# Performance work log

Hardware: AMD Instinct MI355X
Metric: run time of the kernel (lower is better)

The kernel has to match this reference:

```python
import jax, jax.numpy as jnp
import numpy as np

D = 256      # input_dim
SE = 512     # emo seq len
SC = 512     # cause seq len
CKS = 8      # chunksize
KC = 3       # causes per emo utterance


def _linear(k, fi, fo):
    kw, kb = jax.random.split(k)
    bound = 1.0 / np.sqrt(fi)
    w = jax.random.uniform(kw, (fi, fo), jnp.float32, -bound, bound)
    b = jax.random.uniform(kb, (fo,), jnp.float32, -bound, bound)
    return w, b


def setup_inputs() -> dict:
    key = jax.random.key(0)
    ks = jax.random.split(key, 12)
    text_emo = jax.random.normal(ks[0], (SE, 1, D), jnp.float32)
    text_cau = jax.random.normal(ks[1], (SC, 1, D), jnp.float32)
    label_ck = jnp.ones((SE, SC // CKS), jnp.int64 if jax.config.jax_enable_x64 else jnp.int32)
    label3 = jax.random.randint(ks[2], (SE, 1, KC), 0, SC)
    rep_W, rep_b = _linear(ks[3], D, D)
    W_W, W_b = _linear(ks[4], 2 * D, D)
    Wo_W, Wo_b = _linear(ks[5], D, 2)
    # GRU params, torch layout transposed to (in, 3*hidden); gate order r,z,n
    bound = 1.0 / np.sqrt(D)
    gru_Wih = jax.random.uniform(ks[6], (D, 3 * D), jnp.float32, -bound, bound)
    gru_Whh = jax.random.uniform(ks[7], (D, 3 * D), jnp.float32, -bound, bound)
    gru_bih = jax.random.uniform(ks[8], (3 * D,), jnp.float32, -bound, bound)
    gru_bhh = jax.random.uniform(ks[9], (3 * D,), jnp.float32, -bound, bound)
    W3_W, W3_b = _linear(ks[10], 3 * D + 1, D)
    cls_W, cls_b = _linear(ks[11], D, 2)
    return {"text_emo": text_emo, "text_cau": text_cau, "label_ck": label_ck,
            "label3": label3, "chunksize": CKS,
            "rep_W": rep_W, "rep_b": rep_b, "W_W": W_W, "W_b": W_b,
            "Wo_W": Wo_W, "Wo_b": Wo_b,
            "gru_Wih": gru_Wih, "gru_Whh": gru_Whh,
            "gru_bih": gru_bih, "gru_bhh": gru_bhh,
            "W3_W": W3_W, "W3_b": W3_b, "cls_W": cls_W, "cls_b": cls_b}


def reference(text_emo, text_cau, label_ck, label3, chunksize,
              rep_W, rep_b, W_W, W_b, Wo_W, Wo_b,
              gru_Wih, gru_Whh, gru_bih, gru_bhh,
              W3_W, W3_b, cls_W, cls_b):
    d = text_emo.shape[-1]
    # shared representation: relu(Linear)
    te = jax.nn.relu(text_emo @ rep_W + rep_b)   # (SE,1,d)
    tc = jax.nn.relu(text_cau @ rep_W + rep_b)   # (SC,1,d)
    emo = te[:, 0, :]                             # (SE,d) batch==1
    cau = tc[:, 0, :]                             # (SC,d)
    se, sc = emo.shape[0], cau.shape[0]
    C = sc // chunksize
    chunks = cau.reshape(C, chunksize, d)         # torch.split of text_cau

    # GRU over each chunk with zero initial state; take last hidden.
    # (Original re-runs this identically for every emo timestep; math is the same.)
    def gru_last(ch):
        def step(h, x):
            gx = x @ gru_Wih + gru_bih
            gh = h @ gru_Whh + gru_bhh
            xr, xz, xn = jnp.split(gx, 3)
            hr, hz, hn = jnp.split(gh, 3)
            r = jax.nn.sigmoid(xr + hr)
            z = jax.nn.sigmoid(xz + hz)
            n = jnp.tanh(xn + r * hn)
            return (1.0 - z) * n + z * h, None
        h, _ = jax.lax.scan(step, jnp.zeros((d,), ch.dtype), ch)
        return h
    ch_last = jax.vmap(gru_last)(chunks)          # (C,d)

    # phase 2: chunk-level classifier per emo timestep (dropout = identity, eval)
    chunkEmb = jnp.concatenate([
        jnp.broadcast_to(emo[:, None, :], (se, C, d)),
        jnp.broadcast_to(ch_last[None, :, :], (se, C, d))], axis=-1)  # (SE,C,2d)
    hidden = jax.nn.sigmoid(chunkEmb @ W_W + W_b)
    phase2 = jax.nn.log_softmax(hidden @ Wo_W + Wo_b, axis=-1)        # (SE,C,2)

    # phase 3: t_ratio=1 -> idx = label_ck[j]; label_ck all ones selects every
    # chunk, so utt_c == full text_cau for each emo step.
    item2 = jnp.linalg.norm(emo[:, None, :] - cau[None, :, :], axis=-1, keepdims=True)
    delta = jnp.concatenate([
        jnp.broadcast_to(emo[:, None, :], (se, sc, d)),
        jnp.broadcast_to(cau[None, :, :], (se, sc, d)),
        item2,
        emo[:, None, :] * cau[None, :, :]], axis=-1)   # (SE,SC,3d+1)
    h3 = jax.nn.relu(delta @ W3_W + W3_b)
    p = jax.nn.log_softmax(h3 @ cls_W + cls_b, axis=-1)               # (SE,SC,2)

    # label3_out: per emo step, binary cause vector over cause utterances
    lab3 = label3[:, 0, :]                                            # (SE,KC)
    L_cau = jnp.zeros((se, sc), phase2.dtype).at[
        jnp.arange(se)[:, None], lab3].set(1.0)
    return phase2, p, L_cau
```

## Files before the change

kernel.cpp:

```cpp
#include <hip/hip_runtime.h>
#include <hip/hip_bf16.h>
#include <hip/hip_fp16.h>
#include <math.h>

#define D   256
#define SE  512
#define SC  512
#define CKS 8
#define NC  64
#define KC  3

typedef __attribute__((ext_vector_type(8))) short short8_t;
typedef __attribute__((ext_vector_type(4))) float f32x4;
typedef _Float16 h2_t __attribute__((ext_vector_type(2)));
typedef _Float16 h8_t __attribute__((ext_vector_type(8)));

__device__ __forceinline__ float sigmoidf_(float x) { return 1.f / (1.f + __expf(-x)); }
__device__ __forceinline__ short bf16s(float f) {
    union { __hip_bfloat16 h; short s; } u; u.h = __float2bfloat16(f); return u.s;
}
__device__ __forceinline__ float bflo(unsigned int u) {
    union { unsigned int u; float f; } v; v.u = u << 16; return v.f;
}
__device__ __forceinline__ short h16s(float f) {
    union { _Float16 h; short s; } u; u.h = (_Float16)f; return u.s;
}
__device__ __forceinline__ float h16f(short s) {
    union { short s; _Float16 h; } u; u.s = s; return (float)u.h;
}
__device__ __forceinline__ h2_t h2u(unsigned int u) {
    union { unsigned int u; h2_t h; } v; v.u = u; return v.h;
}
__device__ __forceinline__ unsigned int u2h(h2_t h) {
    union { unsigned int u; h2_t h; } v; v.h = h; return v.u;
}
__device__ __forceinline__ float hdot2(h2_t a, h2_t b, float c) {
#if __has_builtin(__builtin_amdgcn_fdot2)
    return __builtin_amdgcn_fdot2(a, b, c, false);
#else
    h2_t p = a * b;
    return c + (float)p[0] + (float)p[1];
#endif
}
#define GLOAD_LDS16(g, l) \
    __builtin_amdgcn_global_load_lds((const __attribute__((address_space(1))) void*)(g), \
                                     (__attribute__((address_space(3))) void*)(l), 16, 0, 0)

__global__ __launch_bounds__(256) void prep_all_kernel(
    const float* __restrict__ W3, const float* __restrict__ Wih,
    const float* __restrict__ Whh, const float* __restrict__ WW,
    const float* __restrict__ repW, const float* __restrict__ clsW,
    short* __restrict__ Bprep, uint2* __restrict__ Wih16, uint2* __restrict__ Whh16,
    float4* __restrict__ WWq, float4* __restrict__ W3q,
    float4* __restrict__ repWq, unsigned int* __restrict__ clsP)
{
    const int b = blockIdx.x, t = threadIdx.x;
    if (b < 32) {
        const int idx = b * 256 + t;
        const int p = idx >> 11, k = (idx >> 3) & 255, G = idx & 7;
        const int dbase = p * 64 + ((G ^ (k & 7)) << 3);
        #pragma unroll
        for (int e = 0; e < 8; ++e)
            Bprep[idx * 8 + e] = h16s(W3[(size_t)(513 + dbase + e) * D + k]);
    } else if (b < 416) {
        const bool ih = (b < 224);
        const int tid = (b - (ih ? 32 : 224)) * 256 + t;
        const float* W = ih ? Wih : Whh;
        const int base = (tid / 768) * 4 * 768 + (tid % 768);
        float f0 = W[base], f1 = W[base + 768], f2 = W[base + 1536], f3 = W[base + 2304];
        __half2 plo = __halves2half2(__float2half_rn(f0), __float2half_rn(f1));
        __half2 phi = __halves2half2(__float2half_rn(f2), __float2half_rn(f3));
        uint2 o; o.x = *(unsigned int*)&plo; o.y = *(unsigned int*)&phi;
        (ih ? Wih16 : Whh16)[tid] = o;
    } else if (b < 672) {
        const bool ww = (b < 544);
        const int tid = (b - (ww ? 416 : 544)) * 256 + t;
        const int h = tid >> 14, rem = tid & 16383, d4 = rem >> 8, k = rem & 255;
        const float* src = (ww ? WW : W3) + (size_t)(h * 256 + 4 * d4) * D + k;
        (ww ? WWq : W3q)[tid] = make_float4(src[0], src[256], src[512], src[768]);
    } else if (b < 736) {
        const int tid = (b - 672) * 256 + t;
        const int d4 = tid >> 8, k = tid & 255;
        const float* src = repW + (size_t)(4 * d4) * D + k;
        repWq[tid] = make_float4(src[0], src[256], src[512], src[768]);
    } else {
        unsigned int c0 = (unsigned int)(unsigned short)bf16s(clsW[t * 2]);
        unsigned int c1 = (unsigned int)(unsigned short)bf16s(clsW[t * 2 + 1]);
        clsP[t] = c0 | (c1 << 16);
    }
}

__global__ __launch_bounds__(256) void rep4_kernel(
    const float* __restrict__ te, const float* __restrict__ tc,
    const float4* __restrict__ repWq, const float* __restrict__ b,
    float* __restrict__ emo, float* __restrict__ cau,
    short* __restrict__ emoH, short* __restrict__ cauH,
    float* __restrict__ se2, float* __restrict__ sc2)
{
    const int r0 = blockIdx.x * 4, t = threadIdx.x;
    const float* X = (r0 < SE) ? (te + (size_t)r0 * D) : (tc + (size_t)(r0 - SE) * D);
    __shared__ __align__(16) float xs[4][D];
    #pragma unroll
    for (int r = 0; r < 4; ++r) xs[r][t] = X[r * D + t];
    __syncthreads();
    float acc0 = 0.f, acc1 = 0.f, acc2 = 0.f, acc3 = 0.f;
    #pragma unroll 8
    for (int q = 0; q < 64; ++q) {
        float4 w = repWq[q * 256 + t];
        float4 x0 = *(const float4*)&xs[0][q * 4];
        float4 x1 = *(const float4*)&xs[1][q * 4];
        float4 x2 = *(const float4*)&xs[2][q * 4];
        float4 x3 = *(const float4*)&xs[3][q * 4];
        acc0 = fmaf(x0.x, w.x, acc0); acc0 = fmaf(x0.y, w.y, acc0); acc0 = fmaf(x0.z, w.z, acc0); acc0 = fmaf(x0.w, w.w, acc0);
        acc1 = fmaf(x1.x, w.x, acc1); acc1 = fmaf(x1.y, w.y, acc1); acc1 = fmaf(x1.z, w.z, acc1); acc1 = fmaf(x1.w, w.w, acc1);
        acc2 = fmaf(x2.x, w.x, acc2); acc2 = fmaf(x2.y, w.y, acc2); acc2 = fmaf(x2.z, w.z, acc2); acc2 = fmaf(x2.w, w.w, acc2);
        acc3 = fmaf(x3.x, w.x, acc3); acc3 = fmaf(x3.y, w.y, acc3); acc3 = fmaf(x3.z, w.z, acc3); acc3 = fmaf(x3.w, w.w, acc3);
    }
    const float bb = b[t];
    float v[4] = {fmaxf(acc0 + bb, 0.f), fmaxf(acc1 + bb, 0.f), fmaxf(acc2 + bb, 0.f), fmaxf(acc3 + bb, 0.f)};
    short hv[4];
    #pragma unroll
    for (int r = 0; r < 4; ++r) hv[r] = h16s(v[r]);
    #pragma unroll
    for (int r = 0; r < 4; ++r) {
        const int row = r0 + r;
        if (row < SE) { emo[(size_t)row * D + t] = v[r]; emoH[(size_t)row * D + t] = hv[r]; }
        else { cau[(size_t)(row - SE) * D + t] = v[r]; cauH[(size_t)(row - SE) * D + t] = hv[r]; }
    }
    __shared__ float rsum[4][4];
    #pragma unroll
    for (int r = 0; r < 4; ++r) {
        const float f = h16f(hv[r]);
        float s = f * f;
        s += __shfl_xor(s, 1);  s += __shfl_xor(s, 2);
        s += __shfl_xor(s, 4);  s += __shfl_xor(s, 8);
        s += __shfl_xor(s, 16); s += __shfl_xor(s, 32);
        if ((t & 63) == 0) rsum[r][t >> 6] = s;
    }
    __syncthreads();
    if (t < 4) {
        const float tot = rsum[t][0] + rsum[t][1] + rsum[t][2] + rsum[t][3];
        const int row = r0 + t;
        if (row < SE) se2[row] = tot; else sc2[row - SE] = tot;
    }
}

__global__ __launch_bounds__(768) void gx2_kernel(
    const float* __restrict__ cau, const uint2* __restrict__ Wih16,
    const float* __restrict__ bih, __half* __restrict__ GX16)
{
    const int r0 = blockIdx.x * 2, t = threadIdx.x;
    __shared__ uint2 xs4[2][64];
    if (t < 128) {
        const int r = t >> 6, c = t & 63;
        float4 v = *(const float4*)&cau[(size_t)(r0 + r) * D + c * 4];
        __half2 plo = __halves2half2(__float2half_rn(v.x), __float2half_rn(v.y));
        __half2 phi = __halves2half2(__float2half_rn(v.z), __float2half_rn(v.w));
        uint2 o; o.x = *(unsigned int*)&plo; o.y = *(unsigned int*)&phi;
        xs4[r][c] = o;
    }
    __syncthreads();
    __half2 a00 = __float2half2_rn(0.f), a01 = __float2half2_rn(0.f);
    __half2 a10 = __float2half2_rn(0.f), a11 = __float2half2_rn(0.f);
    #pragma unroll 8
    for (int q = 0; q < 64; ++q) {
        uint2 w = Wih16[q * 768 + t];
        uint2 x0 = xs4[0][q], x1 = xs4[1][q];
        a00 = __hfma2(*(__half2*)&w.x, *(__half2*)&x0.x, a00);
        a01 = __hfma2(*(__half2*)&w.y, *(__half2*)&x0.y, a01);
        a10 = __hfma2(*(__half2*)&w.x, *(__half2*)&x1.x, a10);
        a11 = __hfma2(*(__half2*)&w.y, *(__half2*)&x1.y, a11);
    }
    const float bi = bih[t];
    float g0 = bi + __low2float(a00) + __high2float(a00) + __low2float(a01) + __high2float(a01);
    float g1 = bi + __low2float(a10) + __high2float(a10) + __low2float(a11) + __high2float(a11);
    GX16[(size_t)r0 * 768 + t] = __float2half_rn(g0);
    GX16[(size_t)(r0 + 1) * 768 + t] = __float2half_rn(g1);
}

__global__ __launch_bounds__(768) void gru_rec_kernel(
    const __half* __restrict__ GX16, const uint2* __restrict__ Whh16,
    const float* __restrict__ bhh, float* __restrict__ ch_last)
{
    const int c = blockIdx.x, t = threadIdx.x;
    __shared__ uint2 hqu[64];
    __shared__ float gh_s[768];
    uint2 wreg[64];
    #pragma unroll
    for (int q = 0; q < 64; ++q) wreg[q] = Whh16[q * 768 + t];
    float h = 0.f;
    if (t < 64) { uint2 z; z.x = 0u; z.y = 0u; hqu[t] = z; }
    __syncthreads();
    const float bh = bhh[t];
    for (int s = 0; s < CKS; ++s) {
        const int row = c * CKS + s;
        __half2 a0 = __float2half2_rn(0.f), a1 = __float2half2_rn(0.f);
        #pragma unroll
        for (int q = 0; q < 64; ++q) {
            uint2 hv = hqu[q];
            a0 = __hfma2(*(__half2*)&wreg[q].x, *(__half2*)&hv.x, a0);
            a1 = __hfma2(*(__half2*)&wreg[q].y, *(__half2*)&hv.y, a1);
        }
        gh_s[t] = bh + __low2float(a0) + __high2float(a0) + __low2float(a1) + __high2float(a1);
        __syncthreads();
        if (t < 256) {
            const float gxr = __half2float(GX16[(size_t)row * 768 + t]);
            const float gxz = __half2float(GX16[(size_t)row * 768 + 256 + t]);
            const float gxn = __half2float(GX16[(size_t)row * 768 + 512 + t]);
            float r = sigmoidf_(gxr + gh_s[t]);
            float z = sigmoidf_(gxz + gh_s[256 + t]);
            float n = tanhf(gxn + r * gh_s[512 + t]);
            h = (1.f - z) * n + z * h;
            float f1 = __shfl_down(h, 1);
            float f2 = __shfl_down(h, 2);
            float f3 = __shfl_down(h, 3);
            if ((t & 3) == 0) {
                __half2 plo = __halves2half2(__float2half_rn(h),  __float2half_rn(f1));
                __half2 phi = __halves2half2(__float2half_rn(f2), __float2half_rn(f3));
                uint2 o; o.x = *(unsigned int*)&plo; o.y = *(unsigned int*)&phi;
                hqu[t >> 2] = o;
            }
        }
        __syncthreads();
    }
    if (t < 256) ch_last[c * D + t] = h;
}

__global__ __launch_bounds__(256) void dual_all4_kernel(
    const float* __restrict__ emo, const float* __restrict__ cau, const float* __restrict__ chl,
    const float4* __restrict__ WWq, const float4* __restrict__ W3q,
    const float* __restrict__ Wb, const float* __restrict__ W3b,
    float* __restrict__ HE, float* __restrict__ HC, float* __restrict__ Ae,
    short* __restrict__ AcB)
{
    const int r0 = blockIdx.x * 4, t = threadIdx.x;
    const float* X; const float4* Wq; float bias;
    int seg;
    if (r0 < 512)       { X = emo + (size_t)r0 * D;          Wq = WWq;         bias = 0.f;    seg = 0; }
    else if (r0 < 576)  { X = chl + (size_t)(r0 - 512) * D;  Wq = WWq + 16384; bias = Wb[t];  seg = 1; }
    else if (r0 < 1088) { X = emo + (size_t)(r0 - 576) * D;  Wq = W3q;         bias = 0.f;    seg = 2; }
    else                { X = cau + (size_t)(r0 - 1088) * D; Wq = W3q + 16384; bias = W3b[t]; seg = 3; }
    __shared__ __align__(16) float xs[4][D];
    #pragma unroll
    for (int r = 0; r < 4; ++r) xs[r][t] = X[r * D + t];
    __syncthreads();
    float a0 = bias, a1 = bias, a2 = bias, a3 = bias;
    #pragma unroll 8
    for (int q = 0; q < 64; ++q) {
        float4 w = Wq[q * 256 + t];
        float4 x0 = *(const float4*)&xs[0][q * 4];
        float4 x1 = *(const float4*)&xs[1][q * 4];
        float4 x2 = *(const float4*)&xs[2][q * 4];
        float4 x3 = *(const float4*)&xs[3][q * 4];
        a0 = fmaf(x0.x, w.x, a0); a0 = fmaf(x0.y, w.y, a0); a0 = fmaf(x0.z, w.z, a0); a0 = fmaf(x0.w, w.w, a0);
        a1 = fmaf(x1.x, w.x, a1); a1 = fmaf(x1.y, w.y, a1); a1 = fmaf(x1.z, w.z, a1); a1 = fmaf(x1.w, w.w, a1);
        a2 = fmaf(x2.x, w.x, a2); a2 = fmaf(x2.y, w.y, a2); a2 = fmaf(x2.z, w.z, a2); a2 = fmaf(x2.w, w.w, a2);
        a3 = fmaf(x3.x, w.x, a3); a3 = fmaf(x3.y, w.y, a3); a3 = fmaf(x3.z, w.z, a3); a3 = fmaf(x3.w, w.w, a3);
    }
    float av[4] = {a0, a1, a2, a3};
    #pragma unroll
    for (int r = 0; r < 4; ++r) {
        const int row = r0 + r;
        if (seg == 0)      HE[(size_t)row * D + t] = av[r];
        else if (seg == 1) HC[(size_t)(row - 512) * D + t] = av[r];
        else if (seg == 2) Ae[(size_t)(row - 576) * D + t] = av[r];
        else               AcB[(size_t)(row - 1088) * D + t] = bf16s(av[r]);
    }
}

__global__ __launch_bounds__(256) void phase2_kernel(
    const float* __restrict__ HE, const float* __restrict__ HC,
    const float* __restrict__ WoW, const float* __restrict__ Wob,
    float* __restrict__ out)
{
    const int i = blockIdx.x, t = threadIdx.x;
    const int c = t >> 2, sub = t & 3;
    __shared__ __align__(16) float he_s[D];
    he_s[t] = HE[(size_t)i * D + t];
    __syncthreads();
    float v0 = 0.f, v1 = 0.f;
    const float* hcRow = HC + (size_t)c * D;
    #pragma unroll 4
    for (int kk = 0; kk < 16; ++kk) {
        const int k4 = sub * 64 + kk * 4;
        float4 he = *(const float4*)&he_s[k4];
        float4 hc = *(const float4*)&hcRow[k4];
        float hk;
        hk = sigmoidf_(he.x + hc.x); { float2 wo = *(const float2*)&WoW[(k4 + 0) * 2]; v0 = fmaf(hk, wo.x, v0); v1 = fmaf(hk, wo.y, v1); }
        hk = sigmoidf_(he.y + hc.y); { float2 wo = *(const float2*)&WoW[(k4 + 1) * 2]; v0 = fmaf(hk, wo.x, v0); v1 = fmaf(hk, wo.y, v1); }
        hk = sigmoidf_(he.z + hc.z); { float2 wo = *(const float2*)&WoW[(k4 + 2) * 2]; v0 = fmaf(hk, wo.x, v0); v1 = fmaf(hk, wo.y, v1); }
        hk = sigmoidf_(he.w + hc.w); { float2 wo = *(const float2*)&WoW[(k4 + 3) * 2]; v0 = fmaf(hk, wo.x, v0); v1 = fmaf(hk, wo.y, v1); }
    }
    v0 += __shfl_xor(v0, 1); v0 += __shfl_xor(v0, 2);
    v1 += __shfl_xor(v1, 1); v1 += __shfl_xor(v1, 2);
    if (sub == 0) {
        float l0 = v0 + Wob[0], l1 = v1 + Wob[1];
        float m = fmaxf(l0, l1);
        float lse = m + __logf(__expf(l0 - m) + __expf(l1 - m));
        float2 o; o.x = l0 - lse; o.y = l1 - lse;
        *(float2*)&out[((size_t)i * NC + c) * 2] = o;
    }
}

__global__ __launch_bounds__(512) void p_kernel(
    const short* __restrict__ emoH, const float* __restrict__ se2, const float* __restrict__ sc2,
    const float* __restrict__ Ae,  const short* __restrict__ AcB,
    const float* __restrict__ wn,  const short* __restrict__ Bprep,
    const short* __restrict__ cauH, const float* __restrict__ clsW,
    float* __restrict__ pp)
{
    const int t = threadIdx.x;
    const int i0 = blockIdx.x * 8;
    const int jt = blockIdx.y >> 1, kh = blockIdx.y & 1;
    const int j0 = jt * 64;
    const int l = t & 63, wave = t >> 6;
    const int hi = l >> 4, lo = l & 15;
    const int wj = wave >> 1, wk = wave & 1;
    const int j_base = wj * 16, k_base = wk * 64;
    const int myj = j0 + j_base + lo;

    __shared__ __align__(16) short B_s[32768];
    __shared__ float part2[64][2][2];

    #pragma unroll
    for (int r = 0; r < 8; ++r) {
        const int g = r * 512 + t;
        const int p = g >> 10, rem = g & 1023;
        GLOAD_LDS16(Bprep + ((size_t)(p * 256 + kh * 128) * 8 + rem) * 8, &B_s[g * 8]);
    }

    int kcol[4]; float wn_r[4], c0_r[4], c1_r[4];
    #pragma unroll
    for (int kf = 0; kf < 4; ++kf) {
        const int kg = kh * 128 + k_base + kf * 16 + lo;
        kcol[kf] = kg;
        wn_r[kf] = wn[kg];
        c0_r[kf] = clsW[kg * 2]; c1_r[kf] = clsW[kg * 2 + 1];
    }
    const int swzf0 = (hi ^ (lo & 7)) << 3;
    const int swzf1 = ((4 + hi) ^ (lo & 7)) << 3;
    const float sc2_l = sc2[myj];
    float Ac_r[4][4];
    #pragma unroll
    for (int q = 0; q < 4; ++q)
        #pragma unroll
        for (int kf = 0; kf < 4; ++kf)
            Ac_r[q][kf] = bflo((unsigned int)(unsigned short)AcB[(size_t)(j0 + j_base + hi * 4 + q) * D + kcol[kf]]);

    uint4 cfr[8];
    #pragma unroll
    for (int s = 0; s < 8; ++s) {
        const int p = s >> 1, df = s & 1;
        cfr[s] = *(const uint4*)&cauH[(size_t)myj * D + p * 64 + (df * 4 + hi) * 8];
    }
    __syncthreads();

    #pragma unroll 1
    for (int ii = 0; ii < 8; ii += 2) {
        __syncthreads();
        f32x4 acc[2][4];
        #pragma unroll
        for (int u = 0; u < 2; ++u)
            #pragma unroll
            for (int kf = 0; kf < 4; ++kf) acc[u][kf] = (f32x4)(0.f);
        float dot0 = 0.f, dot1 = 0.f;

        #pragma unroll
        for (int s = 0; s < 8; ++s) {
            const int p = s >> 1, df = s & 1;
            const uint4 eu0 = *(const uint4*)&emoH[(size_t)(i0 + ii) * D + p * 64 + (df * 4 + hi) * 8];
            const uint4 eu1 = *(const uint4*)&emoH[(size_t)(i0 + ii + 1) * D + p * 64 + (df * 4 + hi) * 8];
            const uint4 cu = cfr[s];
            const h2_t c0 = h2u(cu.x), c1 = h2u(cu.y), c2 = h2u(cu.z), c3 = h2u(cu.w);
            const h2_t a0 = h2u(eu0.x), a1 = h2u(eu0.y), a2 = h2u(eu0.z), a3 = h2u(eu0.w);
            const h2_t b0 = h2u(eu1.x), b1 = h2u(eu1.y), b2 = h2u(eu1.z), b3 = h2u(eu1.w);
            dot0 = hdot2(a0, c0, dot0); dot0 = hdot2(a1, c1, dot0);
            dot0 = hdot2(a2, c2, dot0); dot0 = hdot2(a3, c3, dot0);
            dot1 = hdot2(b0, c0, dot1); dot1 = hdot2(b1, c1, dot1);
            dot1 = hdot2(b2, c2, dot1); dot1 = hdot2(b3, c3, dot1);
            union { uint4 u; h8_t h; } af0, af1;
            af0.u.x = u2h(a0 * c0); af0.u.y = u2h(a1 * c1);
            af0.u.z = u2h(a2 * c2); af0.u.w = u2h(a3 * c3);
            af1.u.x = u2h(b0 * c0); af1.u.y = u2h(b1 * c1);
            af1.u.z = u2h(b2 * c2); af1.u.w = u2h(b3 * c3);
            const int swz = df ? swzf1 : swzf0;
            #pragma unroll
            for (int kf = 0; kf < 4; ++kf) {
                const h8_t bf = *(const h8_t*)&B_s[p * 8192 + (k_base + kf * 16 + lo) * 64 + swz];
                acc[0][kf] = __builtin_amdgcn_mfma_f32_16x16x32_f16(af0.h, bf, acc[0][kf], 0, 0, 0);
                acc[1][kf] = __builtin_amdgcn_mfma_f32_16x16x32_f16(af1.h, bf, acc[1][kf], 0, 0, 0);
            }
        }

        #pragma unroll
        for (int u = 0; u < 2; ++u) {
            const int i = i0 + ii + u;
            float dv = u ? dot1 : dot0;
            dv += __shfl_xor(dv, 16); dv += __shfl_xor(dv, 32);
            const float itv_own = sqrtf(fmaxf(se2[i] + sc2_l - 2.f * dv, 0.f));
            float Ae_r[4];
            #pragma unroll
            for (int kf = 0; kf < 4; ++kf) Ae_r[kf] = Ae[(size_t)i * D + kcol[kf]];
            if (u) __syncthreads();
            #pragma unroll
            for (int q = 0; q < 4; ++q) {
                const int j = j_base + hi * 4 + q;
                const float itv = __shfl(itv_own, hi * 4 + q);
                float sv0 = 0.f, sv1 = 0.f;
                #pragma unroll
                for (int kf = 0; kf < 4; ++kf) {
                    float s = acc[u][kf][q] + Ae_r[kf] + Ac_r[q][kf] + itv * wn_r[kf];
                    float h = fmaxf(s, 0.f);
                    sv0 = fmaf(h, c0_r[kf], sv0); sv1 = fmaf(h, c1_r[kf], sv1);
                }
                sv0 += __shfl_xor(sv0, 1); sv0 += __shfl_xor(sv0, 2);
                sv0 += __shfl_xor(sv0, 4); sv0 += __shfl_xor(sv0, 8);
                sv1 += __shfl_xor(sv1, 1); sv1 += __shfl_xor(sv1, 2);
                sv1 += __shfl_xor(sv1, 4); sv1 += __shfl_xor(sv1, 8);
                if (lo == 0) { part2[j][wk][0] = sv0; part2[j][wk][1] = sv1; }
            }
            __syncthreads();
            if (t < 64) {
                float2 o;
                o.x = part2[t][0][0] + part2[t][1][0];
                o.y = part2[t][0][1] + part2[t][1][1];
                *(float2*)&pp[(((size_t)kh * SE + i) * SC + j0 + t) * 2] = o;
            }
        }
    }
}

__global__ __launch_bounds__(512) void pfin_kernel(
    const float* __restrict__ pp, const float* __restrict__ clsb,
    float* __restrict__ pout)
{
    const int i = blockIdx.x, j = threadIdx.x;
    const float2 a = *(const float2*)&pp[((size_t)i * SC + j) * 2];
    const float2 b = *(const float2*)&pp[(((size_t)SE + i) * SC + j) * 2];
    float s0 = a.x + b.x + clsb[0];
    float s1 = a.y + b.y + clsb[1];
    float m = fmaxf(s0, s1);
    float lse = m + __logf(__expf(s0 - m) + __expf(s1 - m));
    float2 o; o.x = s0 - lse; o.y = s1 - lse;
    *(float2*)&pout[((size_t)i * SC + j) * 2] = o;
}

__global__ __launch_bounds__(128) void lcau_kernel(const int* __restrict__ label3, float* __restrict__ L)
{
    const int row = blockIdx.x, t = threadIdx.x;
    float4 z; z.x = z.y = z.z = z.w = 0.f;
    *(float4*)&L[(size_t)row * SC + t * 4] = z;
    __syncthreads();
    if (t < KC) {
        int j = label3[row * KC + t];
        L[(size_t)row * SC + j] = 1.0f;
    }
}

extern "C" void kernel_launch(void* const* d_in, const int* in_sizes, int n_in,
                              void* d_out, int out_size, void* d_ws, size_t ws_size,
                              hipStream_t stream)
{
    const float* text_emo = (const float*)d_in[0];
    const float* text_cau = (const float*)d_in[1];
    const int*   label3   = (const int*)d_in[3];
    const float* rep_W = (const float*)d_in[5];
    const float* rep_b = (const float*)d_in[6];
    const float* W_W   = (const float*)d_in[7];
    const float* W_b   = (const float*)d_in[8];
    const float* Wo_W  = (const float*)d_in[9];
    const float* Wo_b  = (const float*)d_in[10];
    const float* gWih  = (const float*)d_in[11];
    const float* gWhh  = (const float*)d_in[12];
    const float* gbih  = (const float*)d_in[13];
    const float* gbhh  = (const float*)d_in[14];
    const float* W3_W  = (const float*)d_in[15];
    const float* W3_b  = (const float*)d_in[16];
    const float* cls_W = (const float*)d_in[17];
    const float* cls_b = (const float*)d_in[18];

    float* out        = (float*)d_out;
    float* phase2_out = out;
    float* p_out      = out + SE * NC * 2;
    float* lcau_out   = out + SE * NC * 2 + SE * SC * 2;

    float* ws  = (float*)d_ws;
    float* emo = ws;
    float* cau = emo + 131072;
    float* chl = cau + 131072;
    float* HE  = chl + 16384;
    float* HC  = HE + 131072;
    float* Ae  = HC + 16384;
    float4* WWq = (float4*)(Ae + 131072);
    float4* W3q = WWq + 32768;
    short* AcB   = (short*)(W3q + 32768);
    short* Bprep = AcB + 131072;
    uint2* Wih16 = (uint2*)(Bprep + 65536);
    uint2* Whh16 = Wih16 + 49152;
    float4* repWq = (float4*)(Whh16 + 49152);
    short* cauH = (short*)(repWq + 16384);
    short* emoH = cauH + 131072;
    unsigned int* clsP = (unsigned int*)(emoH + 131072);
    float* pp = (float*)(clsP + 256);
    float* sc2 = pp + 1048576;
    float* se2 = sc2 + 512;
    __half* GX16 = (__half*)HE;

    prep_all_kernel<<<737, 256, 0, stream>>>(W3_W, gWih, gWhh, W_W, rep_W, cls_W,
                                             Bprep, Wih16, Whh16, WWq, W3q, repWq, clsP);
    rep4_kernel<<<256, 256, 0, stream>>>(text_emo, text_cau, repWq, rep_b, emo, cau,
                                         emoH, cauH, se2, sc2);
    gx2_kernel<<<256, 768, 0, stream>>>(cau, Wih16, gbih, GX16);
    gru_rec_kernel<<<NC, 768, 0, stream>>>(GX16, Whh16, gbhh, chl);
    dual_all4_kernel<<<400, 256, 0, stream>>>(emo, cau, chl, WWq, W3q, W_b, W3_b,
                                              HE, HC, Ae, AcB);
    phase2_kernel<<<SE, 256, 0, stream>>>(HE, HC, Wo_W, Wo_b, phase2_out);
    p_kernel<<<dim3(64, 16), 512, 0, stream>>>(emoH, se2, sc2, Ae, AcB, W3_W + 512 * D,
                                               Bprep, cauH, cls_W, pp);
    pfin_kernel<<<SE, 512, 0, stream>>>(pp, cls_b, p_out);
    lcau_kernel<<<SE, 128, 0, stream>>>(label3, lcau_out);
}
```

Before: 172.1 us.

## Process one emo row per p_kernel iteration and fuse L_cau into pfin kernel

The p_kernel main loop now handles one emotion row per iteration instead of two. Each cause fragment's MFMA B-operand load from shared memory therefore feeds one MFMA rather than two, but accumulator registers drop by half. The separate lcau kernel is merged into the log-softmax finalisation kernel, which removes one launch. The order of two FMAs in the rep kernel is also swapped, which slightly changes rounding.

```diff
diff --git a/kernel.cpp b/kernel.cpp
--- a/kernel.cpp
+++ b/kernel.cpp
@@ -114,7 +114,7 @@
         acc0 = fmaf(x0.x, w.x, acc0); acc0 = fmaf(x0.y, w.y, acc0); acc0 = fmaf(x0.z, w.z, acc0); acc0 = fmaf(x0.w, w.w, acc0);
         acc1 = fmaf(x1.x, w.x, acc1); acc1 = fmaf(x1.y, w.y, acc1); acc1 = fmaf(x1.z, w.z, acc1); acc1 = fmaf(x1.w, w.w, acc1);
         acc2 = fmaf(x2.x, w.x, acc2); acc2 = fmaf(x2.y, w.y, acc2); acc2 = fmaf(x2.z, w.z, acc2); acc2 = fmaf(x2.w, w.w, acc2);
-        acc3 = fmaf(x3.x, w.x, acc3); acc3 = fmaf(x3.y, w.y, acc3); acc3 = fmaf(x3.z, w.z, acc3); acc3 = fmaf(x3.w, w.w, acc3);
+        acc3 = fmaf(x3.x, w.x, acc3); acc3 = fmaf(x3.y, w.y, acc3); acc3 = fmaf(x3.w, w.w, acc3); acc3 = fmaf(x3.z, w.z, acc3);
     }
     const float bb = b[t];
     float v[4] = {fmaxf(acc0 + bb, 0.f), fmaxf(acc1 + bb, 0.f), fmaxf(acc2 + bb, 0.f), fmaxf(acc3 + bb, 0.f)};
@@ -356,83 +356,76 @@
     __syncthreads();
 
     #pragma unroll 1
-    for (int ii = 0; ii < 8; ii += 2) {
+    for (int ii = 0; ii < 8; ++ii) {
+        const int i = i0 + ii;
         __syncthreads();
-        f32x4 acc[2][4];
-        #pragma unroll
-        for (int u = 0; u < 2; ++u)
-            #pragma unroll
-            for (int kf = 0; kf < 4; ++kf) acc[u][kf] = (f32x4)(0.f);
-        float dot0 = 0.f, dot1 = 0.f;
+        f32x4 acc[4];
+        #pragma unroll
+        for (int kf = 0; kf < 4; ++kf) acc[kf] = (f32x4)(0.f);
+        float dot = 0.f;
 
         #pragma unroll
         for (int s = 0; s < 8; ++s) {
             const int p = s >> 1, df = s & 1;
-            const uint4 eu0 = *(const uint4*)&emoH[(size_t)(i0 + ii) * D + p * 64 + (df * 4 + hi) * 8];
-            const uint4 eu1 = *(const uint4*)&emoH[(size_t)(i0 + ii + 1) * D + p * 64 + (df * 4 + hi) * 8];
+            const uint4 eu = *(const uint4*)&emoH[(size_t)i * D + p * 64 + (df * 4 + hi) * 8];
             const uint4 cu = cfr[s];
+            const h2_t e0 = h2u(eu.x), e1 = h2u(eu.y), e2 = h2u(eu.z), e3 = h2u(eu.w);
             const h2_t c0 = h2u(cu.x), c1 = h2u(cu.y), c2 = h2u(cu.z), c3 = h2u(cu.w);
-            const h2_t a0 = h2u(eu0.x), a1 = h2u(eu0.y), a2 = h2u(eu0.z), a3 = h2u(eu0.w);
-            const h2_t b0 = h2u(eu1.x), b1 = h2u(eu1.y), b2 = h2u(eu1.z), b3 = h2u(eu1.w);
-            dot0 = hdot2(a0, c0, dot0); dot0 = hdot2(a1, c1, dot0);
-            dot0 = hdot2(a2, c2, dot0); dot0 = hdot2(a3, c3, dot0);
-            dot1 = hdot2(b0, c0, dot1); dot1 = hdot2(b1, c1, dot1);
-            dot1 = hdot2(b2, c2, dot1); dot1 = hdot2(b3, c3, dot1);
-            union { uint4 u; h8_t h; } af0, af1;
-            af0.u.x = u2h(a0 * c0); af0.u.y = u2h(a1 * c1);
-            af0.u.z = u2h(a2 * c2); af0.u.w = u2h(a3 * c3);
-            af1.u.x = u2h(b0 * c0); af1.u.y = u2h(b1 * c1);
-            af1.u.z = u2h(b2 * c2); af1.u.w = u2h(b3 * c3);
+            dot = hdot2(e0, c0, dot);
+            dot = hdot2(e1, c1, dot);
+            dot = hdot2(e2, c2, dot);
+            dot = hdot2(e3, c3, dot);
+            union { uint4 u; h8_t h; } afu;
+            afu.u.x = u2h(e0 * c0);
+            afu.u.y = u2h(e1 * c1);
+            afu.u.z = u2h(e2 * c2);
+            afu.u.w = u2h(e3 * c3);
             const int swz = df ? swzf1 : swzf0;
             #pragma unroll
             for (int kf = 0; kf < 4; ++kf) {
                 const h8_t bf = *(const h8_t*)&B_s[p * 8192 + (k_base + kf * 16 + lo) * 64 + swz];
-                acc[0][kf] = __builtin_amdgcn_mfma_f32_16x16x32_f16(af0.h, bf, acc[0][kf], 0, 0, 0);
-                acc[1][kf] = __builtin_amdgcn_mfma_f32_16x16x32_f16(af1.h, bf, acc[1][kf], 0, 0, 0);
+                acc[kf] = __builtin_amdgcn_mfma_f32_16x16x32_f16(afu.h, bf, acc[kf], 0, 0, 0);
             }
         }
 
-        #pragma unroll
-        for (int u = 0; u < 2; ++u) {
-            const int i = i0 + ii + u;
-            float dv = u ? dot1 : dot0;
-            dv += __shfl_xor(dv, 16); dv += __shfl_xor(dv, 32);
-            const float itv_own = sqrtf(fmaxf(se2[i] + sc2_l - 2.f * dv, 0.f));
-            float Ae_r[4];
+        float dv = dot;
+        dv += __shfl_xor(dv, 16); dv += __shfl_xor(dv, 32);
+        const float itv_own = sqrtf(fmaxf(se2[i] + sc2_l - 2.f * dv, 0.f));
+
+        float Ae_r[4];
+        #pragma unroll
+        for (int kf = 0; kf < 4; ++kf) Ae_r[kf] = Ae[(size_t)i * D + kcol[kf]];
+        #pragma unroll
+        for (int q = 0; q < 4; ++q) {
+            const int j = j_base + hi * 4 + q;
+            const float itv = __shfl(itv_own, hi * 4 + q);
+            float sv0 = 0.f, sv1 = 0.f;
             #pragma unroll
-            for (int kf = 0; kf < 4; ++kf) Ae_r[kf] = Ae[(size_t)i * D + kcol[kf]];
-            if (u) __syncthreads();
-            #pragma unroll
-            for (int q = 0; q < 4; ++q) {
-                const int j = j_base + hi * 4 + q;
-                const float itv = __shfl(itv_own, hi * 4 + q);
-                float sv0 = 0.f, sv1 = 0.f;
-                #pragma unroll
-                for (int kf = 0; kf < 4; ++kf) {
-                    float s = acc[u][kf][q] + Ae_r[kf] + Ac_r[q][kf] + itv * wn_r[kf];
-                    float h = fmaxf(s, 0.f);
-                    sv0 = fmaf(h, c0_r[kf], sv0); sv1 = fmaf(h, c1_r[kf], sv1);
-                }
-                sv0 += __shfl_xor(sv0, 1); sv0 += __shfl_xor(sv0, 2);
-                sv0 += __shfl_xor(sv0, 4); sv0 += __shfl_xor(sv0, 8);
-                sv1 += __shfl_xor(sv1, 1); sv1 += __shfl_xor(sv1, 2);
-                sv1 += __shfl_xor(sv1, 4); sv1 += __shfl_xor(sv1, 8);
-                if (lo == 0) { part2[j][wk][0] = sv0; part2[j][wk][1] = sv1; }
+            for (int kf = 0; kf < 4; ++kf) {
+                float s = acc[kf][q] + Ae_r[kf] + Ac_r[q][kf] + itv * wn_r[kf];
+                float h = fmaxf(s, 0.f);
+                sv0 = fmaf(h, c0_r[kf], sv0); sv1 = fmaf(h, c1_r[kf], sv1);
             }
-            __syncthreads();
-            if (t < 64) {
-                float2 o;
-                o.x = part2[t][0][0] + part2[t][1][0];
-                o.y = part2[t][0][1] + part2[t][1][1];
-                *(float2*)&pp[(((size_t)kh * SE + i) * SC + j0 + t) * 2] = o;
-            }
+            sv0 += __shfl_xor(sv0, 1); sv0 += __shfl_xor(sv0, 2);
+            sv0 += __shfl_xor(sv0, 4); sv0 += __shfl_xor(sv0, 8);
+            sv1 += __shfl_xor(sv1, 1); sv1 += __shfl_xor(sv1, 2);
+            sv1 += __shfl_xor(sv1, 4); sv1 += __shfl_xor(sv1, 8);
+            if (lo == 0) { part2[j][wk][0] = sv0; part2[j][wk][1] = sv1; }
         }
-    }
-}
-
-__global__ __launch_bounds__(512) void pfin_kernel(
+        __syncthreads();
+        if (t < 64) {
+            float2 o;
+            o.x = part2[t][0][0] + part2[t][1][0];
+            o.y = part2[t][0][1] + part2[t][1][1];
+            *(float2*)&pp[(((size_t)kh * SE + i) * SC + j0 + t) * 2] = o;
+        }
+    }
+}
+
+__global__ __launch_bounds__(512) void pfin_lcau_kernel(
     const float* __restrict__ pp, const float* __restrict__ clsb,
-    float* __restrict__ pout)
+    const int* __restrict__ label3,
+    float* __restrict__ pout, float* __restrict__ L)
 {
     const int i = blockIdx.x, j = threadIdx.x;
     const float2 a = *(const float2*)&pp[((size_t)i * SC + j) * 2];
@@ -443,17 +436,14 @@
     float lse = m + __logf(__expf(s0 - m) + __expf(s1 - m));
     float2 o; o.x = s0 - lse; o.y = s1 - lse;
     *(float2*)&pout[((size_t)i * SC + j) * 2] = o;
-}
-
-__global__ __launch_bounds__(128) void lcau_kernel(const int* __restrict__ label3, float* __restrict__ L)
-{
-    const int row = blockIdx.x, t = threadIdx.x;
-    float4 z; z.x = z.y = z.z = z.w = 0.f;
-    *(float4*)&L[(size_t)row * SC + t * 4] = z;
-    __syncthreads();
-    if (t < KC) {
-        int j = label3[row * KC + t];
-        L[(size_t)row * SC + j] = 1.0f;
+    if (j < 128) {
+        float4 z; z.x = z.y = z.z = z.w = 0.f;
+        *(float4*)&L[(size_t)i * SC + j * 4] = z;
+    }
+    __syncthreads();
+    if (j < KC) {
+        int idx = label3[i * KC + j];
+        L[(size_t)i * SC + idx] = 1.0f;
     }
 }
 
@@ -517,6 +507,5 @@
     phase2_kernel<<<SE, 256, 0, stream>>>(HE, HC, Wo_W, Wo_b, phase2_out);
     p_kernel<<<dim3(64, 16), 512, 0, stream>>>(emoH, se2, sc2, Ae, AcB, W3_W + 512 * D,
                                                Bprep, cauH, cls_W, pp);
-    pfin_kernel<<<SE, 512, 0, stream>>>(pp, cls_b, p_out);
-    lcau_kernel<<<SE, 128, 0, stream>>>(label3, lcau_out);
-}
+    pfin_lcau_kernel<<<SE, 512, 0, stream>>>(pp, cls_b, label3, p_out, lcau_out);
+}
```

New measurement: 153.4 us. 10.9% less time.
